# Kernel tuning notes

Hardware: AMD Instinct MI355X
Metric: run time of the kernel (lower is better)

Reference implementation:

```python
import jax, jax.numpy as jnp
import numpy as np

DIM = 2048
N_HEADS = 16
N_KV_HEADS = 8
HEAD_DIM = DIM // N_HEADS  # 128
N_REP = N_HEADS // N_KV_HEADS  # 2
HIDDEN = 4 * DIM  # Project hidden dim
SEQ = 2048
BSZ = 2
ROPE_THETA = 10000.0
NEG_INF = -1e9


def setup_inputs() -> dict:
    key = jax.random.key(0)
    ks = jax.random.split(key, 10)
    s_in = 1.0 / np.sqrt(DIM)
    s_hid = 1.0 / np.sqrt(HIDDEN)
    x = jax.random.normal(ks[0], (BSZ, SEQ, DIM), jnp.float32)
    wq = jax.random.normal(ks[1], (DIM, N_HEADS * HEAD_DIM), jnp.float32) * s_in
    wk_w1 = jax.random.normal(ks[2], (DIM, HIDDEN), jnp.float32) * s_in
    wk_w2 = jax.random.normal(ks[3], (HIDDEN, N_KV_HEADS * HEAD_DIM), jnp.float32) * s_hid
    wk_w3 = jax.random.normal(ks[4], (DIM, HIDDEN), jnp.float32) * s_in
    wv_w1 = jax.random.normal(ks[5], (DIM, HIDDEN), jnp.float32) * s_in
    wv_w2 = jax.random.normal(ks[6], (HIDDEN, N_KV_HEADS * HEAD_DIM), jnp.float32) * s_hid
    wv_w3 = jax.random.normal(ks[7], (DIM, HIDDEN), jnp.float32) * s_in
    wo = jax.random.normal(ks[8], (N_HEADS * HEAD_DIM, DIM), jnp.float32) * s_in
    # RoPE tables: angle[t, j] = t * theta^(-2j/head_dim), j in [0, head_dim/2)
    inv_freq = 1.0 / (ROPE_THETA ** (np.arange(0, HEAD_DIM, 2, dtype=np.float64) / HEAD_DIM))
    ang = np.outer(np.arange(SEQ, dtype=np.float64), inv_freq)
    freqs_cos = jnp.asarray(np.cos(ang), jnp.float32)  # [SEQ, HEAD_DIM//2]
    freqs_sin = jnp.asarray(np.sin(ang), jnp.float32)
    # causal additive mask [1, 1, SEQ, SEQ]
    mask = jnp.triu(jnp.full((SEQ, SEQ), NEG_INF, jnp.float32), k=1)[None, None]
    return {
        "x": x, "wq": wq,
        "wk_w1": wk_w1, "wk_w2": wk_w2, "wk_w3": wk_w3,
        "wv_w1": wv_w1, "wv_w2": wv_w2, "wv_w3": wv_w3,
        "wo": wo, "freqs_cos": freqs_cos, "freqs_sin": freqs_sin,
        "mask": mask, "start_pos": 0,
    }


def _rope(x, cos, sin):
    # x: [b, s, h, d]; pairs (x[2j], x[2j+1]) rotated as complex multiply
    xr = x[..., 0::2]
    xi = x[..., 1::2]
    c = cos[None, :, None, :]
    s = sin[None, :, None, :]
    out_r = xr * c - xi * s
    out_i = xr * s + xi * c
    return jnp.stack([out_r, out_i], axis=-1).reshape(x.shape)


def _project(x, w1, w2, w3):
    # SwiGLU-style projection: w2(silu(x@w1) * (x@w3))
    return (jax.nn.silu(x @ w1) * (x @ w3)) @ w2


def reference(x, wq, wk_w1, wk_w2, wk_w3, wv_w1, wv_w2, wv_w3, wo,
              freqs_cos, freqs_sin, mask, start_pos):
    b, s, _ = x.shape
    q = (x @ wq).reshape(b, s, N_HEADS, HEAD_DIM)
    q = _rope(q, freqs_cos, freqs_sin)
    k = _project(x, wk_w1, wk_w2, wk_w3).reshape(b, s, N_KV_HEADS, HEAD_DIM)
    v = _project(x, wv_w1, wv_w2, wv_w3).reshape(b, s, N_KV_HEADS, HEAD_DIM)
    k = _rope(k, freqs_cos, freqs_sin)
    o_keys, o_values = k, v  # is_training=True path: cache is just current k/v
    # repeat_kv (GQA) -> [b, h, s, d]
    kr = jnp.repeat(k, N_REP, axis=2).transpose(0, 2, 1, 3)
    vr = jnp.repeat(v, N_REP, axis=2).transpose(0, 2, 1, 3)
    qt = q.transpose(0, 2, 1, 3)
    scores = jnp.einsum('bhqd,bhkd->bhqk', qt, kr) / np.sqrt(HEAD_DIM).astype(np.float32)
    scores = scores + mask
    attn = jax.nn.softmax(scores.astype(jnp.float32), axis=-1).astype(qt.dtype)
    out = jnp.einsum('bhqk,bhkd->bhqd', attn, vr)
    out = out.transpose(0, 2, 1, 3).reshape(b, s, N_HEADS * HEAD_DIM)
    return (out @ wo, o_keys, o_values)
```

## Files before the change

### kernel.cpp

```cpp
#include <hip/hip_runtime.h>

typedef unsigned short ushort_t;
typedef __attribute__((ext_vector_type(4))) float f32x4;
typedef __attribute__((ext_vector_type(8))) __bf16 bf16x8;
typedef __attribute__((ext_vector_type(4))) unsigned short ushort4_t;
typedef __attribute__((ext_vector_type(8))) unsigned short ushort8_t;
typedef __attribute__((ext_vector_type(2))) unsigned int u32x2;

#define AS1 __attribute__((address_space(1)))
#define AS3 __attribute__((address_space(3)))

__device__ __forceinline__ float bf2f(ushort_t u) {
  unsigned int v = ((unsigned int)u) << 16;
  return __builtin_bit_cast(float, v);
}
__device__ __forceinline__ ushort_t f2bf(float f) {
  unsigned int u = __builtin_bit_cast(unsigned int, f);
  u += 0x7fffu + ((u >> 16) & 1u);
  return (ushort_t)(u >> 16);
}
__device__ __forceinline__ void storeC(float* p, float v) { *p = v; }
__device__ __forceinline__ void storeC(ushort_t* p, float v) { *p = f2bf(v); }

__global__ __launch_bounds__(256) void cast_f32_bf16(const float* __restrict__ in,
                                                     ushort_t* __restrict__ outp) {
  size_t i = ((size_t)blockIdx.x * 256 + threadIdx.x) * 4;
  f32x4 v = *(const f32x4*)(const void*)&in[i];
  ushort4_t o;
#pragma unroll
  for (int j = 0; j < 4; ++j) o[j] = f2bf(v[j]);
  *(ushort4_t*)(void*)&outp[i] = o;
}

__global__ __launch_bounds__(256) void transpose_cast_b(
    const float* __restrict__ W0, const float* __restrict__ W1,
    const float* __restrict__ W2, const float* __restrict__ W3,
    ushort_t* __restrict__ Wt, int K, int N, long long strT) {
  __shared__ float tile[32][33];
  const int z = blockIdx.z;
  const float* W = (z == 0) ? W0 : (z == 1) ? W1 : (z == 2) ? W2 : W3;
  ushort_t* out = Wt + (size_t)(strT * z);
  int n0 = blockIdx.x * 32, k0 = blockIdx.y * 32;
  int tx = threadIdx.x, ty = threadIdx.y;
#pragma unroll
  for (int i = 0; i < 4; ++i)
    tile[ty + 8 * i][tx] = W[(size_t)(k0 + ty + 8 * i) * N + n0 + tx];
  __syncthreads();
#pragma unroll
  for (int i = 0; i < 4; ++i)
    out[(size_t)(n0 + ty + 8 * i) * K + k0 + tx] = f2bf(tile[tx][ty + 8 * i]);
}

__global__ __launch_bounds__(256) void silu_mul(ushort_t* __restrict__ h1,
                                                const ushort_t* __restrict__ h3) {
  size_t i = ((size_t)blockIdx.x * 256 + threadIdx.x) * 8;
  ushort8_t a = *(const ushort8_t*)(const void*)&h1[i];
  ushort8_t b = *(const ushort8_t*)(const void*)&h3[i];
#pragma unroll
  for (int j = 0; j < 8; ++j) {
    float x = bf2f(a[j]);
    float g = x / (1.0f + __expf(-x));
    a[j] = f2bf(g * bf2f(b[j]));
  }
  *(ushort8_t*)(void*)&h1[i] = a;
}

__global__ __launch_bounds__(256) void reduce_q(const float* __restrict__ part,
                                                ushort_t* __restrict__ qb,
                                                const float* __restrict__ fc,
                                                const float* __restrict__ fs) {
  const float alpha = 0.08838834764831845f;
  int p = blockIdx.x * 256 + threadIdx.x;
  int i = p & 63;
  int row = p >> 10;
  int s = row & 2047;
  size_t src = (size_t)row * 2048 + ((p >> 6) & 15) * 128 + 2 * i;
  float xr = part[src] + part[src + 8388608];
  float xi = part[src + 1] + part[src + 8388609];
  float c = fc[s * 64 + i] * alpha, sn = fs[s * 64 + i] * alpha;
  qb[src] = f2bf(xr * c - xi * sn);
  qb[src + 1] = f2bf(xr * sn + xi * c);
}

__global__ __launch_bounds__(256) void reduce_k(const float* __restrict__ part,
                                                ushort_t* __restrict__ kb,
                                                float* __restrict__ okeys,
                                                const float* __restrict__ fc,
                                                const float* __restrict__ fs) {
  int p = blockIdx.x * 256 + threadIdx.x;
  int i = p & 63;
  int row = p >> 9;
  int s = row & 2047;
  size_t src = (size_t)row * 1024 + ((p >> 6) & 7) * 128 + 2 * i;
  float xr = part[src] + part[src + 4194304] + part[src + 8388608] + part[src + 12582912];
  float xi = part[src + 1] + part[src + 1 + 4194304] + part[src + 1 + 8388608] +
             part[src + 1 + 12582912];
  float c = fc[s * 64 + i], sn = fs[s * 64 + i];
  float orr = xr * c - xi * sn;
  float oi = xr * sn + xi * c;
  kb[src] = f2bf(orr);
  kb[src + 1] = f2bf(oi);
  okeys[src] = orr;
  okeys[src + 1] = oi;
}

__global__ __launch_bounds__(256) void reduce_v(const float* __restrict__ part,
                                                float* __restrict__ ovals,
                                                ushort_t* __restrict__ vbT) {
  __shared__ ushort_t tile[32][33];
  int s0 = blockIdx.x * 32, d0 = blockIdx.y * 32, bk = blockIdx.z;
  int b = bk >> 3, kh = bk & 7;
  int tx = threadIdx.x, ty = threadIdx.y;
#pragma unroll
  for (int i = 0; i < 4; ++i) {
    int s = s0 + ty + 8 * i;
    size_t src = ((size_t)(b * 2048 + s)) * 1024 + kh * 128 + d0 + tx;
    float v = part[src] + part[src + 4194304] + part[src + 8388608] + part[src + 12582912];
    tile[ty + 8 * i][tx] = f2bf(v);
    ovals[src] = v;
  }
  __syncthreads();
#pragma unroll
  for (int i = 0; i < 4; ++i) {
    int d = d0 + ty + 8 * i;
    vbT[((size_t)bk * 128 + d) * 2048 + s0 + tx] = tile[tx][ty + 8 * i];
  }
}

__global__ __launch_bounds__(256) void reduce_wo(const float* __restrict__ part,
                                                 float* __restrict__ outp) {
  size_t i = ((size_t)blockIdx.x * 256 + threadIdx.x) * 4;
  f32x4 a = *(const f32x4*)(const void*)&part[i];
  f32x4 b = *(const f32x4*)(const void*)&part[i + 8388608];
  *(f32x4*)(void*)&outp[i] = a + b;
}

__global__ __launch_bounds__(256) void flash_attn(
    const ushort_t* __restrict__ Q, const ushort_t* __restrict__ Kg,
    const ushort_t* __restrict__ VT, ushort_t* __restrict__ O) {
  __shared__ __align__(16) char smem[81920];
  const int xp = blockIdx.x;
  const int bh = blockIdx.y;
  const int b = bh >> 4, h = bh & 15, kh = h >> 1;
  const int t = threadIdx.x, w = t >> 6, lane = t & 63;
  const int fr = lane & 15, fh = lane >> 4;
  const size_t kelem0 = ((size_t)b * 2048) * 1024 + kh * 128;
  const size_t velem0 = ((size_t)(b * 8 + kh)) * 128 * 2048;
  const size_t qrow0 = (size_t)b * 2048;

  size_t oK[4], oV[4];
#pragma unroll
  for (int qv = 0; qv < 4; ++qv) {
    int row = w * 16 + qv * 4 + (lane >> 4);
    oK[qv] = (size_t)row * 1024 + (((lane & 15) ^ (row & 7)) * 8);
    int rd = w * 32 + qv * 8 + (lane >> 3);
    oV[qv] = (size_t)rd * 2048 + (((lane & 7) ^ (rd & 7)) * 8);
  }

  auto stage = [&](int tile, int buf) {
    const size_t kc = (size_t)tile * 64 * 1024;
    const int vc = tile * 64;
    char* kd = smem + buf * 16384 + w * 4096;
    char* vd = smem + 32768 + buf * 16384 + w * 4096;
#pragma unroll
    for (int qv = 0; qv < 4; ++qv) {
      __builtin_amdgcn_global_load_lds((const AS1 void*)(Kg + kelem0 + kc + oK[qv]),
                                       (AS3 void*)(kd + qv * 1024), 16, 0, 0);
      __builtin_amdgcn_global_load_lds((const AS1 void*)(VT + velem0 + oV[qv] + vc),
                                       (AS3 void*)(vd + qv * 1024), 16, 0, 0);
    }
  };

#pragma unroll 1
  for (int ph = 0; ph < 2; ++ph) {
    const int qi = ph ? (15 - xp) : xp;
    const int qw = qi * 128 + w * 32;
    const int nt = 2 * qi + 2;

    bf16x8 qF[2][4];
#pragma unroll
    for (int qt = 0; qt < 2; ++qt)
#pragma unroll
      for (int i = 0; i < 4; ++i)
        qF[qt][i] = *(const bf16x8*)(const void*)(
            Q + (qrow0 + qw + qt * 16 + fr) * 2048 + h * 128 + i * 32 + fh * 8);

    f32x4 acco[8][2] = {};
    float mrun[2] = {-1e30f, -1e30f};
    float lrun[2] = {0.0f, 0.0f};

    stage(0, 0);
#pragma unroll 1
    for (int tt = 0; tt < nt; ++tt) {
      const int c0 = tt * 64;
      if (tt + 1 < nt) {
        stage(tt + 1, (tt + 1) & 1);
        asm volatile("s_waitcnt vmcnt(8)" ::: "memory");
      } else {
        asm volatile("s_waitcnt vmcnt(0)" ::: "memory");
      }
      __builtin_amdgcn_sched_barrier(0);
      __builtin_amdgcn_s_barrier();
      const char* KL = smem + (tt & 1) * 16384;
      const char* VL = smem + 32768 + (tt & 1) * 16384;
      char* PL = smem + 65536 + w * 4096;
      if (c0 <= qw + 31) {
        f32x4 sacc[2][4] = {};
#pragma unroll
        for (int i = 0; i < 4; ++i)
#pragma unroll
          for (int mt = 0; mt < 4; ++mt) {
            bf16x8 kf = *(const bf16x8*)(const void*)(
                KL + (mt * 16 + fr) * 256 + (((i * 4 + fh) ^ (fr & 7)) * 16));
            sacc[0][mt] = __builtin_amdgcn_mfma_f32_16x16x32_bf16(kf, qF[0][i], sacc[0][mt], 0, 0, 0);
            sacc[1][mt] = __builtin_amdgcn_mfma_f32_16x16x32_bf16(kf, qF[1][i], sacc[1][mt], 0, 0, 0);
          }
        if (c0 + 63 > qw) {
#pragma unroll
          for (int qt = 0; qt < 2; ++qt) {
            int qg = qw + qt * 16 + fr;
#pragma unroll
            for (int mt = 0; mt < 4; ++mt)
#pragma unroll
              for (int j = 0; j < 4; ++j)
                if (c0 + mt * 16 + fh * 4 + j > qg) sacc[qt][mt][j] = -1e30f;
          }
        }
#pragma unroll
        for (int qt = 0; qt < 2; ++qt) {
          float mt_ = -1e30f;
#pragma unroll
          for (int mt = 0; mt < 4; ++mt)
#pragma unroll
            for (int j = 0; j < 4; ++j) mt_ = fmaxf(mt_, sacc[qt][mt][j]);
          mt_ = fmaxf(mt_, __shfl_xor(mt_, 16, 64));
          mt_ = fmaxf(mt_, __shfl_xor(mt_, 32, 64));
          float mnew = fmaxf(mrun[qt], mt_);
          float corr = __expf(mrun[qt] - mnew);
          mrun[qt] = mnew;
          float ps = 0.0f;
          float pv[4][4];
#pragma unroll
          for (int mt = 0; mt < 4; ++mt)
#pragma unroll
            for (int j = 0; j < 4; ++j) {
              float pe = __expf(sacc[qt][mt][j] - mnew);
              pv[mt][j] = pe;
              ps += pe;
            }
          ps += __shfl_xor(ps, 16, 64);
          ps += __shfl_xor(ps, 32, 64);
          lrun[qt] = lrun[qt] * corr + ps;
#pragma unroll
          for (int mt = 0; mt < 4; ++mt) {
            unsigned int u0, u1;
            asm("v_cvt_pk_bf16_f32 %0, %1, %2" : "=v"(u0) : "v"(pv[mt][0]), "v"(pv[mt][1]));
            asm("v_cvt_pk_bf16_f32 %0, %1, %2" : "=v"(u1) : "v"(pv[mt][2]), "v"(pv[mt][3]));
            u32x2 val;
            val[0] = u0;
            val[1] = u1;
            *(u32x2*)(void*)(PL + qt * 2048 + fr * 128 +
                             (((2 * mt + (fh >> 1)) ^ (fr & 7)) * 16) + (fh & 1) * 8) = val;
          }
#pragma unroll
          for (int dt = 0; dt < 8; ++dt) acco[dt][qt] *= corr;
        }
        bf16x8 pf[2][2];
#pragma unroll
        for (int qt = 0; qt < 2; ++qt)
#pragma unroll
          for (int ks = 0; ks < 2; ++ks)
            pf[qt][ks] = *(const bf16x8*)(const void*)(
                PL + qt * 2048 + fr * 128 + (((ks * 4 + fh) ^ (fr & 7)) * 16));
#pragma unroll
        for (int dt = 0; dt < 8; ++dt)
#pragma unroll
          for (int ks = 0; ks < 2; ++ks) {
            bf16x8 vf = *(const bf16x8*)(const void*)(
                VL + (dt * 16 + fr) * 128 + (((ks * 4 + fh) ^ (fr & 7)) * 16));
            acco[dt][0] = __builtin_amdgcn_mfma_f32_16x16x32_bf16(vf, pf[0][ks], acco[dt][0], 0, 0, 0);
            acco[dt][1] = __builtin_amdgcn_mfma_f32_16x16x32_bf16(vf, pf[1][ks], acco[dt][1], 0, 0, 0);
          }
      }
      __builtin_amdgcn_s_barrier();
    }
#pragma unroll
    for (int qt = 0; qt < 2; ++qt) {
      float inv = 1.0f / lrun[qt];
      const size_t rb = (qrow0 + qw + qt * 16 + fr) * 2048 + h * 128;
#pragma unroll
      for (int dt = 0; dt < 8; ++dt) {
        ushort4_t o4;
#pragma unroll
        for (int j = 0; j < 4; ++j) o4[j] = f2bf(acco[dt][qt][j] * inv);
        *(ushort4_t*)(void*)(O + rb + dt * 16 + fh * 4) = o4;
      }
    }
  }
}

template <typename CT>
__global__ __launch_bounds__(512, 2) void gemm256(
    const ushort_t* __restrict__ A, const ushort_t* __restrict__ B,
    CT* __restrict__ C, int K, int lda, int ldb, int ldc,
    int nwgx, int nwg, long long strA, long long strB, long long strC) {
  __shared__ __align__(16) char smem[131072];
  const int bz = blockIdx.y;
  const int bid = blockIdx.x;
  const int swz = (bid & 7) * (nwg >> 3) + (bid >> 3);
  const int r0 = (swz / nwgx) * 256;
  const int c0 = (swz % nwgx) * 256;
  const int t = threadIdx.x, w = t >> 6, lane = t & 63;
  const int wm = w >> 2, wn = w & 3;
  const int fr = lane & 15, fh = lane >> 4;
  const int sl = (fh ^ (fr & 7)) << 4;
  const int ldsw = w * 1024;
  const int srow = t >> 3;
  const int scb = (t & 7) ^ (srow & 7);
  const int NT = K >> 6;
  const ushort_t* gA = A + strA * bz + (size_t)(r0 + srow) * lda + scb * 8;
  const ushort_t* gB = B + strB * bz + (size_t)(c0 + srow) * ldb + scb * 8;

  auto stage = [&](int tile, int isB, int h) {
    const ushort_t* g = isB ? gB : gA;
    const size_t ld = isB ? (size_t)ldb : (size_t)lda;
    char* lp = (char*)smem + (isB ? 65536 : 0) + ((tile & 1) << 15) + (h << 14) + ldsw;
    const ushort_t* src = g + (size_t)(h * 128) * ld + tile * 64;
    __builtin_amdgcn_global_load_lds((const AS1 void*)src, (AS3 void*)lp, 16, 0, 0);
    __builtin_amdgcn_global_load_lds((const AS1 void*)(src + 64 * ld),
                                     (AS3 void*)(lp + 8192), 16, 0, 0);
  };

  f32x4 acc[8][4] = {};

  stage(0, 0, 0); stage(0, 1, 0); stage(0, 0, 1); stage(0, 1, 1);
  asm volatile("s_waitcnt vmcnt(0)" ::: "memory");
  __builtin_amdgcn_sched_barrier(0);
  __builtin_amdgcn_s_barrier();

  const int aBase = wm * 16384 + fr * 128;
  const int bBase = 65536 + wn * 8192 + fr * 128;

  for (int kt = 0; kt < NT; ++kt) {
    const int buf = (kt & 1) << 15;
    const char* la = (const char*)smem + buf + aBase;
    const char* lb = (const char*)smem + buf + bBase;
    bf16x8 aL[4], aH[4], bb[4];
#pragma unroll
    for (int m = 0; m < 4; ++m)
      aL[m] = *(const bf16x8*)(const void*)(la + m * 2048 + sl);
#pragma unroll
    for (int n = 0; n < 4; ++n)
      bb[n] = *(const bf16x8*)(const void*)(lb + n * 2048 + sl);
    if (kt + 1 < NT) { stage(kt + 1, 0, 0); stage(kt + 1, 1, 0); }
    __builtin_amdgcn_s_barrier();
    asm volatile("s_waitcnt lgkmcnt(0)" ::: "memory");
    __builtin_amdgcn_sched_barrier(0);
    __builtin_amdgcn_s_setprio(1);
#pragma unroll
    for (int m = 0; m < 4; ++m)
#pragma unroll
      for (int n = 0; n < 4; ++n)
        acc[m][n] = __builtin_amdgcn_mfma_f32_16x16x32_bf16(aL[m], bb[n], acc[m][n], 0, 0, 0);
    __builtin_amdgcn_s_setprio(0);
    __builtin_amdgcn_s_barrier();
#pragma unroll
    for (int m = 0; m < 4; ++m)
      aH[m] = *(const bf16x8*)(const void*)(la + (m + 4) * 2048 + sl);
    if (kt + 1 < NT) { stage(kt + 1, 0, 1); stage(kt + 1, 1, 1); }
    __builtin_amdgcn_s_barrier();
    asm volatile("s_waitcnt lgkmcnt(0)" ::: "memory");
    __builtin_amdgcn_sched_barrier(0);
    __builtin_amdgcn_s_setprio(1);
#pragma unroll
    for (int m = 0; m < 4; ++m)
#pragma unroll
      for (int n = 0; n < 4; ++n)
        acc[m + 4][n] = __builtin_amdgcn_mfma_f32_16x16x32_bf16(aH[m], bb[n], acc[m + 4][n], 0, 0, 0);
    __builtin_amdgcn_s_setprio(0);
    __builtin_amdgcn_s_barrier();
#pragma unroll
    for (int m = 0; m < 4; ++m)
      aL[m] = *(const bf16x8*)(const void*)(la + m * 2048 + (sl ^ 64));
#pragma unroll
    for (int n = 0; n < 4; ++n)
      bb[n] = *(const bf16x8*)(const void*)(lb + n * 2048 + (sl ^ 64));
    __builtin_amdgcn_s_barrier();
    asm volatile("s_waitcnt lgkmcnt(0)" ::: "memory");
    __builtin_amdgcn_sched_barrier(0);
    __builtin_amdgcn_s_setprio(1);
#pragma unroll
    for (int m = 0; m < 4; ++m)
#pragma unroll
      for (int n = 0; n < 4; ++n)
        acc[m][n] = __builtin_amdgcn_mfma_f32_16x16x32_bf16(aL[m], bb[n], acc[m][n], 0, 0, 0);
    __builtin_amdgcn_s_setprio(0);
    __builtin_amdgcn_s_barrier();
#pragma unroll
    for (int m = 0; m < 4; ++m)
      aH[m] = *(const bf16x8*)(const void*)(la + (m + 4) * 2048 + (sl ^ 64));
    __builtin_amdgcn_s_barrier();
    asm volatile("s_waitcnt lgkmcnt(0)" ::: "memory");
    __builtin_amdgcn_sched_barrier(0);
    __builtin_amdgcn_s_setprio(1);
#pragma unroll
    for (int m = 0; m < 4; ++m)
#pragma unroll
      for (int n = 0; n < 4; ++n)
        acc[m + 4][n] = __builtin_amdgcn_mfma_f32_16x16x32_bf16(aH[m], bb[n], acc[m + 4][n], 0, 0, 0);
    __builtin_amdgcn_s_setprio(0);
    if (kt + 1 < NT)
      asm volatile("s_waitcnt vmcnt(0)" ::: "memory");
    __builtin_amdgcn_sched_barrier(0);
    __builtin_amdgcn_s_barrier();
  }

  CT* gC = C + strC * bz;
  const int cr = r0 + wm * 128 + fh * 4;
  const int cc = c0 + wn * 64 + fr;
#pragma unroll
  for (int m = 0; m < 8; ++m)
#pragma unroll
    for (int n = 0; n < 4; ++n)
#pragma unroll
      for (int j = 0; j < 4; ++j)
        storeC(&gC[(size_t)(cr + m * 16 + j) * ldc + cc + n * 16], acc[m][n][j]);
}

extern "C" void kernel_launch(void* const* d_in, const int* in_sizes, int n_in,
                              void* d_out, int out_size, void* d_ws, size_t ws_size,
                              hipStream_t stream) {
  const float* x = (const float*)d_in[0];
  const float* wq = (const float*)d_in[1];
  const float* wk1 = (const float*)d_in[2];
  const float* wk2 = (const float*)d_in[3];
  const float* wk3 = (const float*)d_in[4];
  const float* wv1 = (const float*)d_in[5];
  const float* wv2 = (const float*)d_in[6];
  const float* wv3 = (const float*)d_in[7];
  const float* wo = (const float*)d_in[8];
  const float* fc = (const float*)d_in[9];
  const float* fs = (const float*)d_in[10];

  float* outp = (float*)d_out;
  float* okeys = outp + 8388608;
  float* ovals = outp + 12582912;

  char* p = (char*)d_ws;
  auto alloc = [&](size_t bytes) {
    char* r = p;
    p += (bytes + 255) & ~(size_t)255;
    return r;
  };
  ushort_t* xb = (ushort_t*)alloc(8388608ull * 2);
  ushort_t* w4T = (ushort_t*)alloc(4ull * 16777216 * 2);
  ushort_t* w2T = (ushort_t*)alloc(2ull * 8388608 * 2);
  ushort_t* wqoT = (ushort_t*)alloc(2ull * 4194304 * 2);
  ushort_t* qb = (ushort_t*)alloc(8388608ull * 2);
  ushort_t* kb = (ushort_t*)alloc(4194304ull * 2);
  ushort_t* vbT = (ushort_t*)alloc(4194304ull * 2);
  ushort_t* ob = (ushort_t*)alloc(8388608ull * 2);
  char* hreg = alloc(134217728ull);
  ushort_t* h1 = (ushort_t*)hreg;
  float* part67 = (float*)(hreg + 67108864);
  float* partQO = (float*)hreg;

  ushort_t* wk1T = w4T;
  ushort_t* wk2T = w2T;
  ushort_t* wv1T = w4T + 2ull * 16777216;
  ushort_t* wv2T = w2T + 8388608;
  ushort_t* wqT = wqoT;
  ushort_t* woT = wqoT + 4194304;

  dim3 tb(32, 8);

  cast_f32_bf16<<<8192, 256, 0, stream>>>(x, xb);
  transpose_cast_b<<<dim3(256, 64, 4), tb, 0, stream>>>(wk1, wk3, wv1, wv3, w4T,
                                                        2048, 8192, 16777216);
  transpose_cast_b<<<dim3(32, 256, 2), tb, 0, stream>>>(wk2, wv2, wk2, wv2, w2T,
                                                        8192, 1024, 8388608);
  transpose_cast_b<<<dim3(64, 64, 2), tb, 0, stream>>>(wq, wo, wq, wo, wqoT,
                                                       2048, 2048, 4194304);

  gemm256<float><<<dim3(128, 2), 512, 0, stream>>>(
      xb, wqT, partQO, 1024, 2048, 2048, 2048, 8, 128, 1024, 1024, 8388608);
  reduce_q<<<16384, 256, 0, stream>>>(partQO, qb, fc, fs);

  gemm256<ushort_t><<<dim3(512, 2), 512, 0, stream>>>(
      xb, wk1T, h1, 2048, 2048, 2048, 8192, 32, 512, 0, 16777216, 33554432);
  silu_mul<<<16384, 256, 0, stream>>>(h1, h1 + 33554432);
  gemm256<float><<<dim3(64, 4), 512, 0, stream>>>(
      h1, wk2T, part67, 2048, 8192, 8192, 1024, 4, 64, 2048, 2048, 4194304);
  reduce_k<<<8192, 256, 0, stream>>>(part67, kb, okeys, fc, fs);

  gemm256<ushort_t><<<dim3(512, 2), 512, 0, stream>>>(
      xb, wv1T, h1, 2048, 2048, 2048, 8192, 32, 512, 0, 16777216, 33554432);
  silu_mul<<<16384, 256, 0, stream>>>(h1, h1 + 33554432);
  gemm256<float><<<dim3(64, 4), 512, 0, stream>>>(
      h1, wv2T, part67, 2048, 8192, 8192, 1024, 4, 64, 2048, 2048, 4194304);
  reduce_v<<<dim3(64, 4, 16), tb, 0, stream>>>(part67, ovals, vbT);

  flash_attn<<<dim3(8, 32), 256, 0, stream>>>(qb, kb, vbT, ob);

  gemm256<float><<<dim3(128, 2), 512, 0, stream>>>(
      ob, woT, partQO, 1024, 2048, 2048, 2048, 8, 128, 1024, 1024, 8388608);
  reduce_wo<<<8192, 256, 0, stream>>>(partQO, outp);

  (void)in_sizes; (void)n_in; (void)out_size; (void)ws_size;
}
```

Before: 1.050 ms.

## Software-pipeline LDS fragment loads in GEMM main loop, drop intra-iteration barriers

Restructures the GEMM inner loop so LDS fragment reads for the next MFMA block are issued before the current MFMA block runs, using double register sets (aX/aY, bX/bY). The first fragments of the next k-tile are prefetched after the single per-tile barrier, and all four global-to-LDS stages are issued together early in the iteration. This removes most of the per-phase s_barrier and lgkmcnt waits that serialized LDS reads with MFMA work. It relies on compiler-inserted waits for correctness and uses more registers.

```diff
diff --git a/kernel.cpp b/kernel.cpp
--- a/kernel.cpp
+++ b/kernel.cpp
@@ -337,82 +337,93 @@
   asm volatile("s_waitcnt vmcnt(0)" ::: "memory");
   __builtin_amdgcn_sched_barrier(0);
   __builtin_amdgcn_s_barrier();
+  __builtin_amdgcn_sched_barrier(0);
 
   const int aBase = wm * 16384 + fr * 128;
   const int bBase = 65536 + wn * 8192 + fr * 128;
+
+  bf16x8 aX[4], aY[4], bX[4], bY[4];
+  {
+    const char* la0 = (const char*)smem + aBase;
+    const char* lb0 = (const char*)smem + bBase;
+#pragma unroll
+    for (int m = 0; m < 4; ++m)
+      aX[m] = *(const bf16x8*)(const void*)(la0 + m * 2048 + sl);
+#pragma unroll
+    for (int n = 0; n < 4; ++n)
+      bX[n] = *(const bf16x8*)(const void*)(lb0 + n * 2048 + sl);
+  }
 
   for (int kt = 0; kt < NT; ++kt) {
     const int buf = (kt & 1) << 15;
     const char* la = (const char*)smem + buf + aBase;
     const char* lb = (const char*)smem + buf + bBase;
-    bf16x8 aL[4], aH[4], bb[4];
-#pragma unroll
-    for (int m = 0; m < 4; ++m)
-      aL[m] = *(const bf16x8*)(const void*)(la + m * 2048 + sl);
-#pragma unroll
-    for (int n = 0; n < 4; ++n)
-      bb[n] = *(const bf16x8*)(const void*)(lb + n * 2048 + sl);
-    if (kt + 1 < NT) { stage(kt + 1, 0, 0); stage(kt + 1, 1, 0); }
-    __builtin_amdgcn_s_barrier();
-    asm volatile("s_waitcnt lgkmcnt(0)" ::: "memory");
+#pragma unroll
+    for (int m = 0; m < 4; ++m)
+      aY[m] = *(const bf16x8*)(const void*)(la + (m + 4) * 2048 + sl);
     __builtin_amdgcn_sched_barrier(0);
     __builtin_amdgcn_s_setprio(1);
 #pragma unroll
     for (int m = 0; m < 4; ++m)
 #pragma unroll
       for (int n = 0; n < 4; ++n)
-        acc[m][n] = __builtin_amdgcn_mfma_f32_16x16x32_bf16(aL[m], bb[n], acc[m][n], 0, 0, 0);
+        acc[m][n] = __builtin_amdgcn_mfma_f32_16x16x32_bf16(aX[m], bX[n], acc[m][n], 0, 0, 0);
     __builtin_amdgcn_s_setprio(0);
-    __builtin_amdgcn_s_barrier();
-#pragma unroll
-    for (int m = 0; m < 4; ++m)
-      aH[m] = *(const bf16x8*)(const void*)(la + (m + 4) * 2048 + sl);
-    if (kt + 1 < NT) { stage(kt + 1, 0, 1); stage(kt + 1, 1, 1); }
-    __builtin_amdgcn_s_barrier();
-    asm volatile("s_waitcnt lgkmcnt(0)" ::: "memory");
+    __builtin_amdgcn_sched_barrier(0);
+#pragma unroll
+    for (int m = 0; m < 4; ++m)
+      aX[m] = *(const bf16x8*)(const void*)(la + m * 2048 + (sl ^ 64));
+#pragma unroll
+    for (int n = 0; n < 4; ++n)
+      bY[n] = *(const bf16x8*)(const void*)(lb + n * 2048 + (sl ^ 64));
+    if (kt + 1 < NT) {
+      stage(kt + 1, 0, 0); stage(kt + 1, 1, 0);
+      stage(kt + 1, 0, 1); stage(kt + 1, 1, 1);
+    }
     __builtin_amdgcn_sched_barrier(0);
     __builtin_amdgcn_s_setprio(1);
 #pragma unroll
     for (int m = 0; m < 4; ++m)
 #pragma unroll
       for (int n = 0; n < 4; ++n)
-        acc[m + 4][n] = __builtin_amdgcn_mfma_f32_16x16x32_bf16(aH[m], bb[n], acc[m + 4][n], 0, 0, 0);
+        acc[m + 4][n] = __builtin_amdgcn_mfma_f32_16x16x32_bf16(aY[m], bX[n], acc[m + 4][n], 0, 0, 0);
     __builtin_amdgcn_s_setprio(0);
-    __builtin_amdgcn_s_barrier();
-#pragma unroll
-    for (int m = 0; m < 4; ++m)
-      aL[m] = *(const bf16x8*)(const void*)(la + m * 2048 + (sl ^ 64));
-#pragma unroll
-    for (int n = 0; n < 4; ++n)
-      bb[n] = *(const bf16x8*)(const void*)(lb + n * 2048 + (sl ^ 64));
-    __builtin_amdgcn_s_barrier();
-    asm volatile("s_waitcnt lgkmcnt(0)" ::: "memory");
+    __builtin_amdgcn_sched_barrier(0);
+#pragma unroll
+    for (int m = 0; m < 4; ++m)
+      aY[m] = *(const bf16x8*)(const void*)(la + (m + 4) * 2048 + (sl ^ 64));
     __builtin_amdgcn_sched_barrier(0);
     __builtin_amdgcn_s_setprio(1);
 #pragma unroll
     for (int m = 0; m < 4; ++m)
 #pragma unroll
       for (int n = 0; n < 4; ++n)
-        acc[m][n] = __builtin_amdgcn_mfma_f32_16x16x32_bf16(aL[m], bb[n], acc[m][n], 0, 0, 0);
+        acc[m][n] = __builtin_amdgcn_mfma_f32_16x16x32_bf16(aX[m], bY[n], acc[m][n], 0, 0, 0);
     __builtin_amdgcn_s_setprio(0);
-    __builtin_amdgcn_s_barrier();
-#pragma unroll
-    for (int m = 0; m < 4; ++m)
-      aH[m] = *(const bf16x8*)(const void*)(la + (m + 4) * 2048 + (sl ^ 64));
-    __builtin_amdgcn_s_barrier();
-    asm volatile("s_waitcnt lgkmcnt(0)" ::: "memory");
     __builtin_amdgcn_sched_barrier(0);
     __builtin_amdgcn_s_setprio(1);
 #pragma unroll
     for (int m = 0; m < 4; ++m)
 #pragma unroll
       for (int n = 0; n < 4; ++n)
-        acc[m + 4][n] = __builtin_amdgcn_mfma_f32_16x16x32_bf16(aH[m], bb[n], acc[m + 4][n], 0, 0, 0);
+        acc[m + 4][n] = __builtin_amdgcn_mfma_f32_16x16x32_bf16(aY[m], bY[n], acc[m + 4][n], 0, 0, 0);
     __builtin_amdgcn_s_setprio(0);
-    if (kt + 1 < NT)
+    if (kt + 1 < NT) {
       asm volatile("s_waitcnt vmcnt(0)" ::: "memory");
-    __builtin_amdgcn_sched_barrier(0);
-    __builtin_amdgcn_s_barrier();
+      __builtin_amdgcn_sched_barrier(0);
+      __builtin_amdgcn_s_barrier();
+      __builtin_amdgcn_sched_barrier(0);
+      const int nbuf = ((kt + 1) & 1) << 15;
+      const char* lan = (const char*)smem + nbuf + aBase;
+      const char* lbn = (const char*)smem + nbuf + bBase;
+#pragma unroll
+      for (int m = 0; m < 4; ++m)
+        aX[m] = *(const bf16x8*)(const void*)(lan + m * 2048 + sl);
+#pragma unroll
+      for (int n = 0; n < 4; ++n)
+        bX[n] = *(const bf16x8*)(const void*)(lbn + n * 2048 + sl);
+      __builtin_amdgcn_sched_barrier(0);
+    }
   }
 
   CT* gC = C + strC * bz;
```

Result: no change. 1.037 ms (-1.3%).
